# Kernel optimization log

Hardware: AMD Instinct MI355X
Metric: run time of the kernel (lower is better)

## Reference

```python
import jax, jax.numpy as jnp
import numpy as np

B, T, L, D, H = 4, 8, 197, 512, 8
DK = D // H
SIM_TH = 0.0
N = T * (L - 1)  # 1568 local tokens

def _ln(x, g, b, eps=1e-5):
    x32 = x.astype(jnp.float32)
    m = jnp.mean(x32, axis=-1, keepdims=True)
    v = jnp.mean((x32 - m) ** 2, axis=-1, keepdims=True)
    return (((x32 - m) * jax.lax.rsqrt(v + eps)) * g + b).astype(x.dtype)

def _qgelu(x):
    return x * jax.nn.sigmoid(1.702 * x)

def _mha(x, w_in, b_in, w_out, b_out):
    # torch nn.MultiheadAttention, x: [S, Bt, D] (seq-first)
    S, Bt, _ = x.shape
    qkv = x @ w_in.T + b_in
    q, k, v = jnp.split(qkv, 3, axis=-1)
    q = q.reshape(S, Bt, H, DK); k = k.reshape(S, Bt, H, DK); v = v.reshape(S, Bt, H, DK)
    scores = jnp.einsum('sbhd,tbhd->bhst', q, k) / jnp.sqrt(jnp.asarray(DK, x.dtype))
    p = jax.nn.softmax(scores, axis=-1)
    o = jnp.einsum('bhst,tbhd->sbhd', p, v).reshape(S, Bt, D)
    return o @ w_out.T + b_out

def _resblock(x, ln1g, ln1b, inw, inb, outw, outb, ln2g, ln2b, fcw, fcb, pw, pb):
    x = x + _mha(_ln(x, ln1g, ln1b), inw, inb, outw, outb)
    h = _qgelu(_ln(x, ln2g, ln2b) @ fcw.T + fcb)
    return x + h @ pw.T + pb

def _build_graph(x, g_mask):
    xd = jax.lax.stop_gradient(x)  # matches x.detach()
    xn = xd / jnp.maximum(jnp.linalg.norm(xd, axis=-1, keepdims=True), 1e-12)
    sim = jnp.einsum('bnd,bmd->bnm', xn, xn)
    adj = jnp.where(sim < SIM_TH, 0.0, sim)
    return adj * g_mask  # t != 1 branch

def _graph_attn(x, mask, wq, bq, wk, bk, wv, bv, wo, bo):
    Bb, Nn, _ = x.shape
    def heads(a):
        return a.reshape(Bb, Nn, H, DK).transpose(0, 2, 1, 3)
    Q = heads(x @ wq.T + bq); K = heads(x @ wk.T + bk); V = heads(x @ wv.T + bv)
    scores = jnp.einsum('bhnd,bhmd->bhnm', Q, K) / jnp.sqrt(jnp.asarray(DK, x.dtype))
    m = mask[:, None]  # [b,1,N,N]
    scores = jnp.where(m == 0, -jnp.inf, scores * m)  # scores*mask then masked_fill(mask==0,-inf)
    p = jax.nn.softmax(scores, axis=-1)
    o = jnp.einsum('bhnm,bhmd->bhnd', p, V).transpose(0, 2, 1, 3).reshape(Bb, Nn, D)
    return o @ wo.T + bo

def _forward(x, proj_w, proj_b,
             m_ln1g, m_ln1b, m_inw, m_inb, m_outw, m_outb,
             m_ln2g, m_ln2b, m_fcw, m_fcb, m_pw, m_pb,
             g_wq, g_bq, g_wk, g_bk, g_wv, g_bv, g_wo, g_bo,
             ln1g, ln1b, a_inw, a_inb, a_outw, a_outb,
             ln2g, ln2b, fcw, fcb, pw, pb, g_mask):
    b, t, l, d = x.shape
    x = x @ proj_w.T + proj_b
    glob = x[:, :, 0, :].transpose(1, 0, 2)  # [t,b,d]
    msg = (m_ln1g, m_ln1b, m_inw, m_inb, m_outw, m_outb, m_ln2g, m_ln2b, m_fcw, m_fcb, m_pw, m_pb)
    glob = _resblock(glob, *msg)
    glob = _resblock(glob, *msg)  # message_attn applied twice (shared weights)
    glob = glob.reshape(1, t, b, d)
    loc = x[:, :, 1:, :].reshape(b, t * (l - 1), d)
    gm = _build_graph(loc, g_mask)
    loc = _graph_attn(loc, gm, g_wq, g_bq, g_wk, g_bk, g_wv, g_bv, g_wo, g_bo)
    loc = loc.reshape(b, t, l - 1, d).transpose(2, 1, 0, 3)  # [l-1,t,b,d]
    y = jnp.concatenate([glob, loc], axis=0).reshape(l, t * b, d)
    y = y + _mha(_ln(y, ln1g, ln1b), a_inw, a_inb, a_outw, a_outb)
    y = y + _qgelu(_ln(y, ln2g, ln2b) @ fcw.T + fcb) @ pw.T + pb
    return y.reshape(l, t, b, d).transpose(2, 1, 0, 3)  # [b,t,l,d]

def setup_inputs() -> dict:
    key = jax.random.key(0)
    ks = jax.random.split(key, 64)
    s = 0.02
    def w(i, shape):
        return jax.random.normal(ks[i], shape, jnp.float32) * s
    ones = jnp.ones((D,), jnp.float32); zeros = jnp.zeros((D,), jnp.float32)
    gm = (jax.random.uniform(ks[60], (N, N)) < 0.5).astype(jnp.float32)
    gm = gm.at[jnp.arange(N), jnp.arange(N)].set(1.0)  # keep self-edges so no row is fully masked
    return dict(
        x=jax.random.normal(ks[0], (B, T, L, D), jnp.float32),
        proj_w=w(1, (D, D)), proj_b=jnp.zeros((D,), jnp.float32),
        m_ln1g=ones, m_ln1b=zeros,
        m_inw=w(2, (3 * D, D)), m_inb=jnp.zeros((3 * D,), jnp.float32),
        m_outw=w(3, (D, D)), m_outb=zeros,
        m_ln2g=ones, m_ln2b=zeros,
        m_fcw=w(4, (4 * D, D)), m_fcb=jnp.zeros((4 * D,), jnp.float32),
        m_pw=w(5, (D, 4 * D)), m_pb=zeros,
        g_wq=w(6, (D, D)), g_bq=zeros, g_wk=w(7, (D, D)), g_bk=zeros,
        g_wv=w(8, (D, D)), g_bv=zeros, g_wo=w(9, (D, D)), g_bo=zeros,
        ln1g=ones, ln1b=zeros,
        a_inw=w(10, (3 * D, D)), a_inb=jnp.zeros((3 * D,), jnp.float32),
        a_outw=w(11, (D, D)), a_outb=zeros,
        ln2g=ones, ln2b=zeros,
        fcw=w(12, (4 * D, D)), fcb=jnp.zeros((4 * D,), jnp.float32),
        pw=w(13, (D, 4 * D)), pb=zeros,
        g_mask=gm,
    )

def reference(x, proj_w, proj_b, m_ln1g, m_ln1b, m_inw, m_inb, m_outw, m_outb,
              m_ln2g, m_ln2b, m_fcw, m_fcb, m_pw, m_pb,
              g_wq, g_bq, g_wk, g_bk, g_wv, g_bv, g_wo, g_bo,
              ln1g, ln1b, a_inw, a_inb, a_outw, a_outb,
              ln2g, ln2b, fcw, fcb, pw, pb, g_mask):
    return _forward(x, proj_w, proj_b, m_ln1g, m_ln1b, m_inw, m_inb, m_outw, m_outb,
                    m_ln2g, m_ln2b, m_fcw, m_fcb, m_pw, m_pb,
                    g_wq, g_bq, g_wk, g_bk, g_wv, g_bv, g_wo, g_bo,
                    ln1g, ln1b, a_inw, a_inb, a_outw, a_outb,
                    ln2g, ln2b, fcw, fcb, pw, pb, g_mask)
```

## Files before the change

kernel.cpp:

```cpp
#include <hip/hip_runtime.h>
#include <hip/hip_bf16.h>

typedef unsigned short u16;
typedef __attribute__((ext_vector_type(8))) short bf16x8;
typedef __attribute__((ext_vector_type(4))) float f32x4;

#define FINF __builtin_huge_valf()

static __device__ __forceinline__ float bf2f(u16 v){ union{unsigned u; float f;} c; c.u = ((unsigned)v)<<16; return c.f; }
static __device__ __forceinline__ u16 f2bf(float f){ union{__hip_bfloat16 h; u16 u;} c; c.h = __float2bfloat16(f); return c.u; }

static __device__ __forceinline__ void gload16(const void* g, void* l){
  __builtin_amdgcn_global_load_lds(
      (const __attribute__((address_space(1))) void*)g,
      (__attribute__((address_space(3))) void*)l, 16, 0, 0);
}

#define WAIT_VM0()   { asm volatile("s_waitcnt vmcnt(0)" ::: "memory"); __builtin_amdgcn_sched_barrier(0); }
#define WAIT_LGKM0() { asm volatile("s_waitcnt lgkmcnt(0)" ::: "memory"); __builtin_amdgcn_sched_barrier(0); }
#define BARRIER()    { __builtin_amdgcn_sched_barrier(0); __builtin_amdgcn_s_barrier(); __builtin_amdgcn_sched_barrier(0); }

struct CvtArgs {
  const float* src[14];
  u16* dst[14];
  int n[14];
};
__global__ __launch_bounds__(256) void cvt_multi(CvtArgs a){
  int seg = blockIdx.y;
  const float* s = a.src[seg]; u16* d = a.dst[seg]; int n = a.n[seg];
  for (int i = (blockIdx.x*256 + threadIdx.x)*4; i < n; i += gridDim.x*256*4){
    float4 v = *(const float4*)(s + i);
    ushort4 o = { f2bf(v.x), f2bf(v.y), f2bf(v.z), f2bf(v.w) };
    *(ushort4*)(d + i) = o;
  }
}

__global__ __launch_bounds__(256) void concat_bias(const float* a, const float* b, const float* c, float* o){
  int i = blockIdx.x*256 + threadIdx.x;
  o[i] = i < 512 ? a[i] : (i < 1024 ? b[i-512] : c[i-1024]);
}

template<int BM, int EPI>
__global__ __launch_bounds__(256,2) void gemm_nt(
    const u16* __restrict__ A, const u16* __restrict__ Bw,
    const float* __restrict__ bias, const float* aux, void* out,
    int M, int Nn, int K, int ldc, long aBatch, long bBatch, long cBatch)
{
  constexpr int MI = BM/32;
  constexpr int WSPAN = BM/2;
  __shared__ __align__(16) u16 a_lds[2*BM*64];
  __shared__ __align__(16) u16 b_lds[2*128*64];
  const int z = blockIdx.z;
  const u16* Az = A + (long)z*aBatch;
  const u16* Bz = Bw + (long)z*bBatch;
  const int n0 = blockIdx.x*128, m0 = blockIdx.y*BM;
  const int t = threadIdx.x, lane = t & 63, wave = t >> 6;
  const int wr = wave >> 1, wc = wave & 1;
  const int r = lane & 15, kq = lane >> 4;

  const int srow = t >> 3;
  const int scol = ((t&7)*8) ^ ((srow&7)<<3);
  int rowA[MI], rowB[4];
  #pragma unroll
  for (int i=0;i<MI;i++){ int ga = m0 + i*32 + srow; rowA[i] = ga < M ? ga : M-1; }
  #pragma unroll
  for (int i=0;i<4;i++){ int gb = n0 + i*32 + srow; rowB[i] = gb < Nn ? gb : Nn-1; }

  f32x4 acc[MI][4] = {};
  const int nkt = K >> 6;

  auto STAGE = [&](int kt, int buf){
    const long koff = (long)kt*64 + scol;
    #pragma unroll
    for (int i=0;i<MI;i++)
      gload16(Az + (long)rowA[i]*K + koff, (char*)a_lds + buf*(BM*128) + i*4096 + wave*1024);
    #pragma unroll
    for (int i=0;i<4;i++)
      gload16(Bz + (long)rowB[i]*K + koff, (char*)b_lds + buf*16384 + i*4096 + wave*1024);
  };

  STAGE(0,0);
  WAIT_VM0(); BARRIER();
  for (int kt=0; kt<nkt; kt++){
    const int cur = kt&1;
    if (kt+1 < nkt) STAGE(kt+1, cur^1);
    const u16* al = a_lds + cur*BM*64;
    const u16* bl = b_lds + cur*8192;
    #pragma unroll
    for (int kk=0; kk<2; kk++){
      bf16x8 af[MI], bfr[4];
      #pragma unroll
      for (int i=0;i<MI;i++){
        int rw = wr*WSPAN + i*16 + r;
        af[i] = *(const bf16x8*)&al[rw*64 + ((kk*32 + kq*8) ^ ((rw&7)<<3))];
      }
      #pragma unroll
      for (int j=0;j<4;j++){
        int rw = wc*64 + j*16 + r;
        bfr[j] = *(const bf16x8*)&bl[rw*64 + ((kk*32 + kq*8) ^ ((rw&7)<<3))];
      }
      #pragma unroll
      for (int i=0;i<MI;i++)
        #pragma unroll
        for (int j=0;j<4;j++)
          acc[i][j] = __builtin_amdgcn_mfma_f32_16x16x32_bf16(af[i], bfr[j], acc[i][j], 0,0,0);
    }
    WAIT_VM0(); BARRIER();
  }

  #pragma unroll
  for (int i=0;i<MI;i++){
    #pragma unroll
    for (int j=0;j<4;j++){
      int gcol = n0 + wc*64 + j*16 + r;
      if (gcol >= Nn) continue;
      float bv = bias ? bias[gcol] : 0.f;
      #pragma unroll
      for (int rr=0; rr<4; rr++){
        int grow = m0 + wr*WSPAN + i*16 + kq*4 + rr;
        if (grow >= M) continue;
        float v = acc[i][j][rr] + bv;
        if constexpr (EPI==0){
          ((float*)out)[(long)z*cBatch + (long)grow*ldc + gcol] = v;
        } else if constexpr (EPI==1){
          ((u16*)out)[(long)z*cBatch + (long)grow*ldc + gcol] = f2bf(v);
        } else if constexpr (EPI==2){
          long idx = (long)z*cBatch + (long)grow*ldc + gcol;
          ((float*)out)[idx] = aux[idx] + v;
        } else if constexpr (EPI==3){
          float g = v / (1.f + __expf(-1.702f*v));
          ((u16*)out)[(long)z*cBatch + (long)grow*ldc + gcol] = f2bf(g);
        } else if constexpr (EPI==4){
          float adj = v < 0.f ? 0.f : v;
          float gmv = aux[(long)grow*Nn + gcol];
          ((u16*)out)[(long)z*cBatch + (long)grow*ldc + gcol] = f2bf(adj*gmv);
        } else if constexpr (EPI==5){
          int b = grow/1568, n = grow%1568, tt = n/196, lp = n%196;
          int yrow = (1+lp)*32 + tt*4 + b;
          ((float*)out)[(long)yrow*ldc + gcol] = v;
        } else if constexpr (EPI==6){
          long idx = (long)grow*ldc + gcol;
          int l = grow>>5, rb = grow&31, tt = rb>>2, bb = rb&3;
          ((float*)out)[((long)((bb*8+tt)*197) + l)*512 + gcol] = aux[idx] + v;
        }
      }
    }
  }
}

template<bool MASKED>
__global__ __launch_bounds__(256,2) void flash_attn(
    const u16* __restrict__ QKV, const u16* __restrict__ gmask, u16* __restrict__ Out,
    int nq, int nk, long qBatch, long qRow, long oBatch, long oRow, long gmBatch)
{
  __shared__ __align__(16) u16 k_lds[2][4096];
  __shared__ __align__(16) u16 vt[2][64*74];
  __shared__ __align__(16) u16 gt[MASKED?2:1][MASKED?64*70:4];
  __shared__ __align__(16) u16 p_lds[4][16*72];
  const int h = blockIdx.y, z = blockIdx.z;
  const int t = threadIdx.x, lane = t&63, wave = t>>6;
  const int r = lane&15, kq = lane>>4;
  const u16* Qb = QKV + (long)z*qBatch + h*64;
  const u16* Kb = Qb + 512;
  const u16* Vb = Qb + 1024;
  const u16* Gz = gmask + (long)z*gmBatch;
  const int qt0 = blockIdx.x*64;
  const int q0 = qt0 + wave*16;

  bf16x8 qf0, qf1;
  {
    int qi = q0 + r; if (qi > nq-1) qi = nq-1;
    const u16* qp = Qb + (long)qi*qRow + kq*8;
    qf0 = *(const bf16x8*)qp;
    qf1 = *(const bf16x8*)(qp + 32);
  }

  const int srow = t>>3;
  const int scol = ((t&7)*8) ^ ((srow&7)<<3);

  uint4 vv[2]; uint4 gv[2];

  auto stage_k = [&](int kt, int buf){
    #pragma unroll
    for (int i=0;i<2;i++){
      int j = kt*64 + i*32 + srow; if (j > nk-1) j = nk-1;
      gload16(Kb + (long)j*qRow + scol, (char*)&k_lds[buf][0] + i*4096 + wave*1024);
    }
  };
  auto load_v = [&](int kt){
    #pragma unroll
    for (int i=0;i<2;i++){
      int c = i*256 + t; int vj = kt*64 + (c>>3); if (vj > nk-1) vj = nk-1;
      vv[i] = *(const uint4*)(Vb + (long)vj*qRow + (c&7)*8);
    }
  };
  auto load_g = [&](int kt){
    #pragma unroll
    for (int i=0;i<2;i++){
      int c = i*256 + t; int qr = qt0 + (c>>3); if (qr > nq-1) qr = nq-1;
      gv[i] = *(const uint4*)(Gz + (long)qr*nk + kt*64 + (c&7)*8);
    }
  };
  auto write_vt = [&](int buf){
    #pragma unroll
    for (int i=0;i<2;i++){
      int c = i*256 + t; int vrow = c>>3, cc = (c&7)*8;
      #pragma unroll
      for (int e=0;e<8;e++) vt[buf][(cc+e)*74 + vrow] = ((const u16*)&vv[i])[e];
    }
  };
  auto write_gt = [&](int buf){
    #pragma unroll
    for (int i=0;i<2;i++){
      int c = i*256 + t; int qlr = c>>3, cc = (c&7)*8;
      #pragma unroll
      for (int e=0;e<8;e++) gt[buf][(cc+e)*70 + qlr] = ((const u16*)&gv[i])[e];
    }
  };

  float m_[4] = {-FINF,-FINF,-FINF,-FINF};
  float l_[4] = {0,0,0,0};
  f32x4 o_[4] = {};

  const int nkt = (nk + 63) >> 6;
  stage_k(0,0); load_v(0);
  if constexpr (MASKED) load_g(0);
  WAIT_VM0(); BARRIER();

  for (int kt=0; kt<nkt; kt++){
    const int cur = kt&1;
    write_vt(cur);
    if constexpr (MASKED) write_gt(cur);
    if (kt+1 < nkt){
      stage_k(kt+1, cur^1);
      load_v(kt+1);
      if constexpr (MASKED) load_g(kt+1);
    }
    WAIT_LGKM0(); BARRIER();

    float s[4][4];
    #pragma unroll
    for (int sub=0; sub<4; sub++){
      int rw = sub*16 + r; int sw = (rw&7)<<3;
      bf16x8 kf0 = *(const bf16x8*)&k_lds[cur][rw*64 + ((kq*8) ^ sw)];
      bf16x8 kf1 = *(const bf16x8*)&k_lds[cur][rw*64 + ((32 + kq*8) ^ sw)];
      f32x4 sc = {};
      sc = __builtin_amdgcn_mfma_f32_16x16x32_bf16(qf0, kf0, sc, 0,0,0);
      sc = __builtin_amdgcn_mfma_f32_16x16x32_bf16(qf1, kf1, sc, 0,0,0);
      #pragma unroll
      for (int rr=0;rr<4;rr++) s[sub][rr] = sc[rr];
    }
    #pragma unroll
    for (int sub=0; sub<4; sub++){
      int key = kt*64 + sub*16 + r;
      bool kdead = key >= nk;
      #pragma unroll
      for (int rr=0;rr<4;rr++){
        float sv = s[sub][rr]*0.125f;
        if constexpr (MASKED){
          int lrow = wave*16 + kq*4 + rr;
          u16 g = gt[cur][(sub*16+r)*70 + lrow];
          if (g == 0 || kdead) sv = -FINF; else sv *= bf2f(g);
        } else {
          if (kdead) sv = -FINF;
        }
        s[sub][rr] = sv;
      }
    }
    #pragma unroll
    for (int rr=0;rr<4;rr++){
      float mx = fmaxf(fmaxf(s[0][rr],s[1][rr]), fmaxf(s[2][rr],s[3][rr]));
      #pragma unroll
      for (int d=1; d<16; d<<=1) mx = fmaxf(mx, __shfl_xor(mx, d));
      float mnew = fmaxf(m_[rr], mx);
      float fac = (m_[rr] == -FINF) ? 0.f : __expf(m_[rr] - mnew);
      float ps = 0.f;
      #pragma unroll
      for (int sub=0;sub<4;sub++){
        float p = (s[sub][rr] == -FINF) ? 0.f : __expf(s[sub][rr] - mnew);
        s[sub][rr] = p; ps += p;
      }
      #pragma unroll
      for (int d=1; d<16; d<<=1) ps += __shfl_xor(ps, d);
      l_[rr] = l_[rr]*fac + ps;
      m_[rr] = mnew;
      o_[0][rr]*=fac; o_[1][rr]*=fac; o_[2][rr]*=fac; o_[3][rr]*=fac;
    }
    #pragma unroll
    for (int rr=0;rr<4;rr++){
      int prow = kq*4+rr;
      #pragma unroll
      for (int sub=0;sub<4;sub++)
        p_lds[wave][prow*72 + ((sub*16+r) ^ ((prow&7)<<3))] = f2bf(s[sub][rr]);
    }
    #pragma unroll
    for (int c=0;c<2;c++){
      bf16x8 pf = *(const bf16x8*)&p_lds[wave][r*72 + ((c*32 + kq*8) ^ ((r&7)<<3))];
      #pragma unroll
      for (int j=0;j<4;j++){
        bf16x8 vf = *(const bf16x8*)&vt[cur][(j*16+r)*74 + c*32 + kq*8];
        o_[j] = __builtin_amdgcn_mfma_f32_16x16x32_bf16(pf, vf, o_[j], 0,0,0);
      }
    }
    WAIT_VM0(); BARRIER();
  }

  #pragma unroll
  for (int rr=0;rr<4;rr++){
    int qrow = q0 + kq*4 + rr;
    if (qrow >= nq) continue;
    float inv = l_[rr] > 0.f ? 1.f/l_[rr] : 0.f;
    #pragma unroll
    for (int j=0;j<4;j++)
      Out[(long)z*oBatch + (long)qrow*oRow + h*64 + j*16 + r] = f2bf(o_[j][rr]*inv);
  }
}

__global__ __launch_bounds__(256) void ln_rows(const float* __restrict__ in,
    const float* __restrict__ g, const float* __restrict__ b, u16* __restrict__ out, int rows)
{
  int wave = threadIdx.x >> 6, lane = threadIdx.x & 63;
  int row = blockIdx.x*4 + wave;
  if (row >= rows) return;
  const float4* x = (const float4*)(in + (long)row*512);
  float4 v0 = x[lane], v1 = x[lane+64];
  float s  = v0.x+v0.y+v0.z+v0.w + v1.x+v1.y+v1.z+v1.w;
  float ss = v0.x*v0.x+v0.y*v0.y+v0.z*v0.z+v0.w*v0.w + v1.x*v1.x+v1.y*v1.y+v1.z*v1.z+v1.w*v1.w;
  #pragma unroll
  for (int d=1; d<64; d<<=1){ s += __shfl_xor(s,d); ss += __shfl_xor(ss,d); }
  float mean = s * (1.f/512.f);
  float var = ss * (1.f/512.f) - mean*mean;
  float rs = rsqrtf(var + 1e-5f);
  const float4* gg = (const float4*)g; const float4* bb = (const float4*)b;
  float4 g0 = gg[lane], g1 = gg[lane+64], b0 = bb[lane], b1 = bb[lane+64];
  u16* o = out + (long)row*512;
  ushort4 o0 = { f2bf((v0.x-mean)*rs*g0.x + b0.x), f2bf((v0.y-mean)*rs*g0.y + b0.y),
                 f2bf((v0.z-mean)*rs*g0.z + b0.z), f2bf((v0.w-mean)*rs*g0.w + b0.w) };
  ushort4 o1 = { f2bf((v1.x-mean)*rs*g1.x + b1.x), f2bf((v1.y-mean)*rs*g1.y + b1.y),
                 f2bf((v1.z-mean)*rs*g1.z + b1.z), f2bf((v1.w-mean)*rs*g1.w + b1.w) };
  *(ushort4*)(o + lane*4) = o0;
  *(ushort4*)(o + 256 + lane*4) = o1;
}

__global__ __launch_bounds__(256) void locprep(const float* __restrict__ y0,
    u16* __restrict__ xn, u16* __restrict__ locb)
{
  int wave = threadIdx.x >> 6, lane = threadIdx.x & 63;
  int rr = blockIdx.x*4 + wave;
  int bb = rr/1568, n = rr%1568, tt = n/196, lp = n%196;
  const float4* x = (const float4*)(y0 + ((long)((bb*8+tt)*197) + 1 + lp)*512);
  float4 v0 = x[lane], v1 = x[lane+64];
  float ss = v0.x*v0.x+v0.y*v0.y+v0.z*v0.z+v0.w*v0.w + v1.x*v1.x+v1.y*v1.y+v1.z*v1.z+v1.w*v1.w;
  #pragma unroll
  for (int d=1; d<64; d<<=1) ss += __shfl_xor(ss,d);
  float sc = 1.f / fmaxf(sqrtf(ss), 1e-12f);
  u16* ox = xn + (long)rr*512;
  u16* ol = locb + (long)rr*512;
  ushort4 a0 = { f2bf(v0.x*sc), f2bf(v0.y*sc), f2bf(v0.z*sc), f2bf(v0.w*sc) };
  ushort4 a1 = { f2bf(v1.x*sc), f2bf(v1.y*sc), f2bf(v1.z*sc), f2bf(v1.w*sc) };
  ushort4 c0 = { f2bf(v0.x), f2bf(v0.y), f2bf(v0.z), f2bf(v0.w) };
  ushort4 c1 = { f2bf(v1.x), f2bf(v1.y), f2bf(v1.z), f2bf(v1.w) };
  *(ushort4*)(ox + lane*4) = a0;  *(ushort4*)(ox + 256 + lane*4) = a1;
  *(ushort4*)(ol + lane*4) = c0;  *(ushort4*)(ol + 256 + lane*4) = c1;
}

__global__ __launch_bounds__(64) void msg_attn(const u16* __restrict__ mqkv, u16* __restrict__ matt){
  __shared__ float q_s[8][64], k_s[8][64], v_s[8][64];
  int bh = blockIdx.x; int bt = bh>>3, h = bh&7;
  int lane = threadIdx.x;
  int row = lane>>3, cc = (lane&7)*8;
  #pragma unroll
  for (int e=0;e<8;e++){
    long base = (long)(row*4 + bt)*1536 + h*64 + cc + e;
    q_s[row][cc+e] = bf2f(mqkv[base]);
    k_s[row][cc+e] = bf2f(mqkv[base + 512]);
    v_s[row][cc+e] = bf2f(mqkv[base + 1024]);
  }
  __syncthreads();
  int q = lane>>3, k = lane&7;
  float s = 0.f;
  #pragma unroll 16
  for (int d=0; d<64; d++) s += q_s[q][d]*k_s[k][d];
  s *= 0.125f;
  float mx = s;
  #pragma unroll
  for (int d=1; d<8; d<<=1) mx = fmaxf(mx, __shfl_xor(mx,d));
  float p = __expf(s - mx), ps = p;
  #pragma unroll
  for (int d=1; d<8; d<<=1) ps += __shfl_xor(ps,d);
  p /= ps;
  for (int d=0; d<64; d++){
    float ov = p * v_s[k][d];
    #pragma unroll
    for (int m=1; m<8; m<<=1) ov += __shfl_xor(ov,m);
    if (k == (d>>3)) matt[(long)(q*4 + bt)*512 + h*64 + d] = f2bf(ov);
  }
}

__global__ __launch_bounds__(256) void gather_glob(const float* __restrict__ y0, float* __restrict__ glob){
  int idx = blockIdx.x*256 + threadIdx.x;
  int orow = idx>>9, d = idx&511;
  int tt = orow>>2, bb = orow&3;
  glob[idx] = y0[((long)(bb*8+tt)*197)*512 + d];
}
__global__ __launch_bounds__(256) void copy32(const float* __restrict__ glob, float* __restrict__ y){
  int idx = blockIdx.x*256 + threadIdx.x;
  y[idx] = glob[idx];
}

extern "C" void kernel_launch(void* const* d_in, const int* in_sizes, int n_in,
                              void* d_out, int out_size, void* d_ws, size_t ws_size,
                              hipStream_t stream)
{
  const float* x      = (const float*)d_in[0];
  const float* proj_w = (const float*)d_in[1];
  const float* proj_b = (const float*)d_in[2];
  const float* m_ln1g = (const float*)d_in[3];
  const float* m_ln1b = (const float*)d_in[4];
  const float* m_inw  = (const float*)d_in[5];
  const float* m_inb  = (const float*)d_in[6];
  const float* m_outw = (const float*)d_in[7];
  const float* m_outb = (const float*)d_in[8];
  const float* m_ln2g = (const float*)d_in[9];
  const float* m_ln2b = (const float*)d_in[10];
  const float* m_fcw  = (const float*)d_in[11];
  const float* m_fcb  = (const float*)d_in[12];
  const float* m_pw   = (const float*)d_in[13];
  const float* m_pb   = (const float*)d_in[14];
  const float* g_wq = (const float*)d_in[15]; const float* g_bq = (const float*)d_in[16];
  const float* g_wk = (const float*)d_in[17]; const float* g_bk = (const float*)d_in[18];
  const float* g_wv = (const float*)d_in[19]; const float* g_bv = (const float*)d_in[20];
  const float* g_wo = (const float*)d_in[21]; const float* g_bo = (const float*)d_in[22];
  const float* ln1g = (const float*)d_in[23]; const float* ln1b = (const float*)d_in[24];
  const float* a_inw = (const float*)d_in[25]; const float* a_inb = (const float*)d_in[26];
  const float* a_outw = (const float*)d_in[27]; const float* a_outb = (const float*)d_in[28];
  const float* ln2g = (const float*)d_in[29]; const float* ln2b = (const float*)d_in[30];
  const float* fcw = (const float*)d_in[31]; const float* fcb = (const float*)d_in[32];
  const float* pw = (const float*)d_in[33]; const float* pb = (const float*)d_in[34];
  const float* g_mask = (const float*)d_in[35];

  if (ws_size < (size_t)99753984) return;

  char* ws = (char*)d_ws;
  u16* WB = (u16*)ws;
  const long WPROJ=0, WMIN=262144, WMOUT=1048576, WMFC=1310720, WMP=2359296,
             WGQ=3407872, WGK=3670016, WGV=3932160, WGO=4194304,
             WAIN=4456448, WAOUT=5242880, WFC=5505024, WP=6553600;
  float* y0   = (float*)(ws + 15204352);
  float* y    = (float*)(ws + 28114944);
  u16* lnbuf  = (u16*)(ws + 41025536);
  u16* locb   = (u16*)(ws + 47480832);
  u16* qkv    = (u16*)(ws + 53903360);
  u16* xb     = (u16*)(ws + 73269248);
  u16* gm     = (u16*)(ws + 73269248);
  u16* hbuf   = (u16*)(ws + 73269248);
  u16* obuf   = (u16*)(ws + 92938240);
  float* glob = (float*)(ws + 99393536);
  u16* mlnb   = (u16*)(ws + 99459072);
  u16* mqkv   = (u16*)(ws + 99491840);
  u16* matt   = (u16*)(ws + 99590144);
  u16* mh     = (u16*)(ws + 99622912);
  float* gbias = (float*)(ws + 99622912);

  CvtArgs ca;
  auto setseg=[&](int i, const float* s, u16* d, int n){ ca.src[i]=s; ca.dst[i]=d; ca.n[i]=n; };
  setseg(0,  x,      xb,       6304*512);
  setseg(1,  proj_w, WB+WPROJ, 262144);
  setseg(2,  m_inw,  WB+WMIN,  786432);
  setseg(3,  m_outw, WB+WMOUT, 262144);
  setseg(4,  m_fcw,  WB+WMFC,  1048576);
  setseg(5,  m_pw,   WB+WMP,   1048576);
  setseg(6,  g_wq,   WB+WGQ,   262144);
  setseg(7,  g_wk,   WB+WGK,   262144);
  setseg(8,  g_wv,   WB+WGV,   262144);
  setseg(9,  g_wo,   WB+WGO,   262144);
  setseg(10, a_inw,  WB+WAIN,  786432);
  setseg(11, a_outw, WB+WAOUT, 262144);
  setseg(12, fcw,    WB+WFC,   1048576);
  setseg(13, pw,     WB+WP,    1048576);
  cvt_multi<<<dim3(128,14), 256, 0, stream>>>(ca);

  gemm_nt<64,0><<<dim3(4,99), 256, 0, stream>>>(xb, WB+WPROJ, proj_b, nullptr, y0, 6304,512,512,512, 0,0,0);

  gather_glob<<<64,256,0,stream>>>(y0, glob);

  for (int it=0; it<2; ++it){
    ln_rows<<<8,256,0,stream>>>(glob, m_ln1g, m_ln1b, mlnb, 32);
    gemm_nt<64,1><<<dim3(12,1),256,0,stream>>>(mlnb, WB+WMIN, m_inb, nullptr, mqkv, 32,1536,512,1536, 0,0,0);
    msg_attn<<<32,64,0,stream>>>(mqkv, matt);
    gemm_nt<64,2><<<dim3(4,1),256,0,stream>>>(matt, WB+WMOUT, m_outb, glob, glob, 32,512,512,512, 0,0,0);
    ln_rows<<<8,256,0,stream>>>(glob, m_ln2g, m_ln2b, mlnb, 32);
    gemm_nt<64,3><<<dim3(16,1),256,0,stream>>>(mlnb, WB+WMFC, m_fcb, nullptr, mh, 32,2048,512,2048, 0,0,0);
    gemm_nt<64,2><<<dim3(4,1),256,0,stream>>>(mh, WB+WMP, m_pb, glob, glob, 32,512,2048,512, 0,0,0);
  }

  concat_bias<<<6,256,0,stream>>>(g_bq, g_bk, g_bv, gbias);

  locprep<<<1568,256,0,stream>>>(y0, lnbuf, locb);

  gemm_nt<128,4><<<dim3(13,13,4),256,0,stream>>>(lnbuf, lnbuf, nullptr, g_mask, gm,
      1568,1568,512,1568, 1568L*512, 1568L*512, 1568L*1568);

  gemm_nt<128,1><<<dim3(12,49),256,0,stream>>>(locb, WB+WGQ, gbias, nullptr, qkv, 6272,1536,512,1536, 0,0,0);

  flash_attn<true><<<dim3(25,8,4),256,0,stream>>>(qkv, gm, obuf,
      1568,1568, 1568L*1536, 1536, 1568L*512, 512, 1568L*1568);

  gemm_nt<64,5><<<dim3(4,98),256,0,stream>>>(obuf, WB+WGO, g_bo, nullptr, y, 6272,512,512,512, 0,0,0);

  copy32<<<64,256,0,stream>>>(glob, y);

  ln_rows<<<1576,256,0,stream>>>(y, ln1g, ln1b, lnbuf, 6304);
  gemm_nt<128,1><<<dim3(12,50),256,0,stream>>>(lnbuf, WB+WAIN, a_inb, nullptr, qkv, 6304,1536,512,1536, 0,0,0);
  flash_attn<false><<<dim3(4,8,32),256,0,stream>>>(qkv, nullptr, obuf,
      197,197, 1536, 32L*1536, 512, 32L*512, 0);
  gemm_nt<64,2><<<dim3(4,99),256,0,stream>>>(obuf, WB+WAOUT, a_outb, y, y, 6304,512,512,512, 0,0,0);

  ln_rows<<<1576,256,0,stream>>>(y, ln2g, ln2b, lnbuf, 6304);
  gemm_nt<128,3><<<dim3(16,50),256,0,stream>>>(lnbuf, WB+WFC, fcb, nullptr, hbuf, 6304,2048,512,2048, 0,0,0);
  gemm_nt<64,6><<<dim3(4,99),256,0,stream>>>(hbuf, WB+WP, pb, y, (float*)d_out, 6304,512,2048,512, 0,0,0);
}
```

Measured before the change: 649.7 us.

## Widen flash attention to 128-query tiles with 8 waves and async mask staging

The flash attention kernel now uses 512 threads covering 128 query rows per block, so each K/V tile staged in LDS is reused by twice as many queries. The graph mask is loaded straight into swizzled LDS with global_load_lds instead of a register-transposed write, and V is kept in a single swizzled buffer. Q is pre-scaled by 1/8 at load time, and the softmax row sums come from an extra MFMA against a ones vector instead of shuffle reductions. This cuts redundant K/V traffic and shuffle work, at the cost of fewer blocks and more padded query rows for the short 197-token attention.

```diff
diff --git a/kernel.cpp b/kernel.cpp
--- a/kernel.cpp
+++ b/kernel.cpp
@@ -9,6 +9,12 @@
 
 static __device__ __forceinline__ float bf2f(u16 v){ union{unsigned u; float f;} c; c.u = ((unsigned)v)<<16; return c.f; }
 static __device__ __forceinline__ u16 f2bf(float f){ union{__hip_bfloat16 h; u16 u;} c; c.h = __float2bfloat16(f); return c.u; }
+static __device__ __forceinline__ bf16x8 scale8(bf16x8 v, float s){
+  bf16x8 o;
+  #pragma unroll
+  for (int e=0;e<8;e++) o[e] = (short)f2bf(bf2f((u16)v[e])*s);
+  return o;
+}
 
 static __device__ __forceinline__ void gload16(const void* g, void* l){
   __builtin_amdgcn_global_load_lds(
@@ -17,7 +23,6 @@
 }
 
 #define WAIT_VM0()   { asm volatile("s_waitcnt vmcnt(0)" ::: "memory"); __builtin_amdgcn_sched_barrier(0); }
-#define WAIT_LGKM0() { asm volatile("s_waitcnt lgkmcnt(0)" ::: "memory"); __builtin_amdgcn_sched_barrier(0); }
 #define BARRIER()    { __builtin_amdgcn_sched_barrier(0); __builtin_amdgcn_s_barrier(); __builtin_amdgcn_sched_barrier(0); }
 
 struct CvtArgs {
@@ -149,101 +154,83 @@
 }
 
 template<bool MASKED>
-__global__ __launch_bounds__(256,2) void flash_attn(
+__global__ __launch_bounds__(512,4) void flash_attn(
     const u16* __restrict__ QKV, const u16* __restrict__ gmask, u16* __restrict__ Out,
     int nq, int nk, long qBatch, long qRow, long oBatch, long oRow, long gmBatch)
 {
-  __shared__ __align__(16) u16 k_lds[2][4096];
-  __shared__ __align__(16) u16 vt[2][64*74];
-  __shared__ __align__(16) u16 gt[MASKED?2:1][MASKED?64*70:4];
-  __shared__ __align__(16) u16 p_lds[4][16*72];
-  const int h = blockIdx.y, z = blockIdx.z;
+  __shared__ __align__(16) u16 k_lds[2*4096];
+  __shared__ __align__(16) u16 vt[64*72];
+  __shared__ __align__(16) u16 p_lds[8][16*72];
+  __shared__ __align__(16) u16 g_lds[MASKED ? 2*8192 : 8];
   const int t = threadIdx.x, lane = t&63, wave = t>>6;
   const int r = lane&15, kq = lane>>4;
+  const int h = blockIdx.y, z = blockIdx.z;
   const u16* Qb = QKV + (long)z*qBatch + h*64;
   const u16* Kb = Qb + 512;
   const u16* Vb = Qb + 1024;
   const u16* Gz = gmask + (long)z*gmBatch;
-  const int qt0 = blockIdx.x*64;
-  const int q0 = qt0 + wave*16;
+  const int qt0 = blockIdx.x*128;
+  const int q0  = qt0 + wave*16;
 
   bf16x8 qf0, qf1;
-  {
-    int qi = q0 + r; if (qi > nq-1) qi = nq-1;
+  { int qi = q0 + r; if (qi > nq-1) qi = nq-1;
     const u16* qp = Qb + (long)qi*qRow + kq*8;
-    qf0 = *(const bf16x8*)qp;
-    qf1 = *(const bf16x8*)(qp + 32);
-  }
+    qf0 = scale8(*(const bf16x8*)qp, 0.125f);
+    qf1 = scale8(*(const bf16x8*)(qp+32), 0.125f); }
 
   const int srow = t>>3;
   const int scol = ((t&7)*8) ^ ((srow&7)<<3);
-
-  uint4 vv[2]; uint4 gv[2];
-
+  const int vcc  = (t&7)*8;
+
+  uint4 vv;
   auto stage_k = [&](int kt, int buf){
+    int j = kt*64 + srow; if (j > nk-1) j = nk-1;
+    gload16(Kb + (long)j*qRow + scol, (char*)k_lds + buf*8192 + wave*1024);
+  };
+  auto stage_g = [&](int kt, int buf){
     #pragma unroll
     for (int i=0;i<2;i++){
-      int j = kt*64 + i*32 + srow; if (j > nk-1) j = nk-1;
-      gload16(Kb + (long)j*qRow + scol, (char*)&k_lds[buf][0] + i*4096 + wave*1024);
+      int qr = qt0 + i*64 + srow; if (qr > nq-1) qr = nq-1;
+      gload16(Gz + (long)qr*nk + kt*64 + scol, (char*)g_lds + buf*16384 + i*8192 + wave*1024);
     }
   };
   auto load_v = [&](int kt){
-    #pragma unroll
-    for (int i=0;i<2;i++){
-      int c = i*256 + t; int vj = kt*64 + (c>>3); if (vj > nk-1) vj = nk-1;
-      vv[i] = *(const uint4*)(Vb + (long)vj*qRow + (c&7)*8);
-    }
+    int vj = kt*64 + srow; if (vj > nk-1) vj = nk-1;
+    vv = *(const uint4*)(Vb + (long)vj*qRow + vcc);
   };
-  auto load_g = [&](int kt){
-    #pragma unroll
-    for (int i=0;i<2;i++){
-      int c = i*256 + t; int qr = qt0 + (c>>3); if (qr > nq-1) qr = nq-1;
-      gv[i] = *(const uint4*)(Gz + (long)qr*nk + kt*64 + (c&7)*8);
-    }
+  auto write_vt = [&](){
+    #pragma unroll
+    for (int e=0;e<8;e++)
+      vt[(vcc+e)*72 + (srow ^ (e<<3))] = ((const u16*)&vv)[e];
   };
-  auto write_vt = [&](int buf){
-    #pragma unroll
-    for (int i=0;i<2;i++){
-      int c = i*256 + t; int vrow = c>>3, cc = (c&7)*8;
-      #pragma unroll
-      for (int e=0;e<8;e++) vt[buf][(cc+e)*74 + vrow] = ((const u16*)&vv[i])[e];
-    }
-  };
-  auto write_gt = [&](int buf){
-    #pragma unroll
-    for (int i=0;i<2;i++){
-      int c = i*256 + t; int qlr = c>>3, cc = (c&7)*8;
-      #pragma unroll
-      for (int e=0;e<8;e++) gt[buf][(cc+e)*70 + qlr] = ((const u16*)&gv[i])[e];
-    }
-  };
+
+  bf16x8 ONES;
+  #pragma unroll
+  for (int e=0;e<8;e++) ONES[e] = (short)0x3F80;
 
   float m_[4] = {-FINF,-FINF,-FINF,-FINF};
-  float l_[4] = {0,0,0,0};
-  f32x4 o_[4] = {};
+  f32x4 o_[4] = {}; f32x4 ol = {};
 
   const int nkt = (nk + 63) >> 6;
-  stage_k(0,0); load_v(0);
-  if constexpr (MASKED) load_g(0);
-  WAIT_VM0(); BARRIER();
-
+  stage_k(0,0); if (MASKED) stage_g(0,0); load_v(0);
+  __syncthreads();
   for (int kt=0; kt<nkt; kt++){
     const int cur = kt&1;
-    write_vt(cur);
-    if constexpr (MASKED) write_gt(cur);
+    write_vt();
+    __syncthreads();
     if (kt+1 < nkt){
       stage_k(kt+1, cur^1);
+      if (MASKED) stage_g(kt+1, cur^1);
       load_v(kt+1);
-      if constexpr (MASKED) load_g(kt+1);
-    }
-    WAIT_LGKM0(); BARRIER();
+    }
 
     float s[4][4];
+    const u16* kl = k_lds + cur*4096;
     #pragma unroll
     for (int sub=0; sub<4; sub++){
       int rw = sub*16 + r; int sw = (rw&7)<<3;
-      bf16x8 kf0 = *(const bf16x8*)&k_lds[cur][rw*64 + ((kq*8) ^ sw)];
-      bf16x8 kf1 = *(const bf16x8*)&k_lds[cur][rw*64 + ((32 + kq*8) ^ sw)];
+      bf16x8 kf0 = *(const bf16x8*)&kl[rw*64 + ((kq*8) ^ sw)];
+      bf16x8 kf1 = *(const bf16x8*)&kl[rw*64 + ((32 + kq*8) ^ sw)];
       f32x4 sc = {};
       sc = __builtin_amdgcn_mfma_f32_16x16x32_bf16(qf0, kf0, sc, 0,0,0);
       sc = __builtin_amdgcn_mfma_f32_16x16x32_bf16(qf1, kf1, sc, 0,0,0);
@@ -256,10 +243,10 @@
       bool kdead = key >= nk;
       #pragma unroll
       for (int rr=0;rr<4;rr++){
-        float sv = s[sub][rr]*0.125f;
+        float sv = s[sub][rr];
         if constexpr (MASKED){
           int lrow = wave*16 + kq*4 + rr;
-          u16 g = gt[cur][(sub*16+r)*70 + lrow];
+          u16 g = g_lds[cur*8192 + lrow*64 + ((sub*16+r) ^ ((lrow&7)<<3))];
           if (g == 0 || kdead) sv = -FINF; else sv *= bf2f(g);
         } else {
           if (kdead) sv = -FINF;
@@ -274,17 +261,11 @@
       for (int d=1; d<16; d<<=1) mx = fmaxf(mx, __shfl_xor(mx, d));
       float mnew = fmaxf(m_[rr], mx);
       float fac = (m_[rr] == -FINF) ? 0.f : __expf(m_[rr] - mnew);
-      float ps = 0.f;
-      #pragma unroll
-      for (int sub=0;sub<4;sub++){
-        float p = (s[sub][rr] == -FINF) ? 0.f : __expf(s[sub][rr] - mnew);
-        s[sub][rr] = p; ps += p;
-      }
-      #pragma unroll
-      for (int d=1; d<16; d<<=1) ps += __shfl_xor(ps, d);
-      l_[rr] = l_[rr]*fac + ps;
+      #pragma unroll
+      for (int sub=0;sub<4;sub++)
+        s[sub][rr] = (s[sub][rr] == -FINF) ? 0.f : __expf(s[sub][rr] - mnew);
       m_[rr] = mnew;
-      o_[0][rr]*=fac; o_[1][rr]*=fac; o_[2][rr]*=fac; o_[3][rr]*=fac;
+      o_[0][rr]*=fac; o_[1][rr]*=fac; o_[2][rr]*=fac; o_[3][rr]*=fac; ol[rr]*=fac;
     }
     #pragma unroll
     for (int rr=0;rr<4;rr++){
@@ -298,18 +279,19 @@
       bf16x8 pf = *(const bf16x8*)&p_lds[wave][r*72 + ((c*32 + kq*8) ^ ((r&7)<<3))];
       #pragma unroll
       for (int j=0;j<4;j++){
-        bf16x8 vf = *(const bf16x8*)&vt[cur][(j*16+r)*74 + c*32 + kq*8];
+        bf16x8 vf = *(const bf16x8*)&vt[(j*16+r)*72 + ((c*32 + kq*8) ^ ((r&7)<<3))];
         o_[j] = __builtin_amdgcn_mfma_f32_16x16x32_bf16(pf, vf, o_[j], 0,0,0);
       }
-    }
-    WAIT_VM0(); BARRIER();
+      ol = __builtin_amdgcn_mfma_f32_16x16x32_bf16(pf, ONES, ol, 0,0,0);
+    }
+    __syncthreads();
   }
 
   #pragma unroll
   for (int rr=0;rr<4;rr++){
     int qrow = q0 + kq*4 + rr;
     if (qrow >= nq) continue;
-    float inv = l_[rr] > 0.f ? 1.f/l_[rr] : 0.f;
+    float inv = ol[rr] > 0.f ? 1.f/ol[rr] : 0.f;
     #pragma unroll
     for (int j=0;j<4;j++)
       Out[(long)z*oBatch + (long)qrow*oRow + h*64 + j*16 + r] = f2bf(o_[j][rr]*inv);
@@ -503,7 +485,7 @@
 
   gemm_nt<128,1><<<dim3(12,49),256,0,stream>>>(locb, WB+WGQ, gbias, nullptr, qkv, 6272,1536,512,1536, 0,0,0);
 
-  flash_attn<true><<<dim3(25,8,4),256,0,stream>>>(qkv, gm, obuf,
+  flash_attn<true><<<dim3(13,8,4),512,0,stream>>>(qkv, gm, obuf,
       1568,1568, 1568L*1536, 1536, 1568L*512, 512, 1568L*1568);
 
   gemm_nt<64,5><<<dim3(4,98),256,0,stream>>>(obuf, WB+WGO, g_bo, nullptr, y, 6272,512,512,512, 0,0,0);
@@ -512,7 +494,7 @@
 
   ln_rows<<<1576,256,0,stream>>>(y, ln1g, ln1b, lnbuf, 6304);
   gemm_nt<128,1><<<dim3(12,50),256,0,stream>>>(lnbuf, WB+WAIN, a_inb, nullptr, qkv, 6304,1536,512,1536, 0,0,0);
-  flash_attn<false><<<dim3(4,8,32),256,0,stream>>>(qkv, nullptr, obuf,
+  flash_attn<false><<<dim3(2,8,32),512,0,stream>>>(qkv, nullptr, obuf,
       197,197, 1536, 32L*1536, 512, 32L*512, 0);
   gemm_nt<64,2><<<dim3(4,99),256,0,stream>>>(obuf, WB+WAOUT, a_outb, y, y, 6304,512,512,512, 0,0,0);
 
```

Measured after the change: 612.8 us. 1.06x faster.
